# Optimization experiments

Measured on AMD Instinct MI355X. Metric: run time of the kernel, lower is better.

Reference implementation:

```python
import jax, jax.numpy as jnp
import numpy as np
import math

N = 20000      # nodes
E = 640000     # edges (avg degree 32)
G = 128        # g_dim (input features)
H1 = 128       # rgcn output dim
H2 = 128       # transformer output dim
R = 8          # num_relations


def setup_inputs() -> dict:
    key = jax.random.key(0)
    ks = jax.random.split(key, 12)
    x = jax.random.normal(ks[0], (N, G), dtype=jnp.float32)
    edge_index = jax.random.randint(ks[1], (2, E), 0, N)
    edge_type = jax.random.randint(ks[2], (E,), 0, R)
    s_in = 1.0 / math.sqrt(G)
    s_h1 = 1.0 / math.sqrt(H1)
    return {
        'x': x,
        'edge_index': edge_index,
        'edge_type': edge_type,
        # RGCNConv params (per-relation weights + root weight + bias)
        'rgcn_weight': jax.random.normal(ks[3], (R, G, H1), dtype=jnp.float32) * s_in,
        'rgcn_root': jax.random.normal(ks[4], (G, H1), dtype=jnp.float32) * s_in,
        'rgcn_bias': jnp.zeros((H1,), dtype=jnp.float32),
        # TransformerConv params (heads=1): query/key/value + skip linear
        'Wq': jax.random.normal(ks[5], (H1, H2), dtype=jnp.float32) * s_h1,
        'bq': jnp.zeros((H2,), dtype=jnp.float32),
        'Wk': jax.random.normal(ks[6], (H1, H2), dtype=jnp.float32) * s_h1,
        'bk': jnp.zeros((H2,), dtype=jnp.float32),
        'Wv': jax.random.normal(ks[7], (H1, H2), dtype=jnp.float32) * s_h1,
        'bv': jnp.zeros((H2,), dtype=jnp.float32),
        'Ws': jax.random.normal(ks[8], (H1, H2), dtype=jnp.float32) * s_h1,
        'bs': jnp.zeros((H2,), dtype=jnp.float32),
    }


def reference(x, edge_index, edge_type, rgcn_weight, rgcn_root, rgcn_bias,
              Wq, bq, Wk, bk, Wv, bv, Ws, bs):
    n = x.shape[0]
    src, dst = edge_index[0], edge_index[1]

    # ---- RGCNConv (aggr='mean' per relation, root weight + bias) ----
    # transform nodes by every relation, then gather per-edge message
    xr = jnp.einsum('ni,rio->nro', x, rgcn_weight)          # [N, R, H1]
    msg = xr[src, edge_type]                                # [E, H1]
    # per (dst, relation) edge counts for mean aggregation
    cnt = jnp.zeros((n, rgcn_weight.shape[0]), x.dtype).at[dst, edge_type].add(1.0)
    denom = jnp.maximum(cnt[dst, edge_type], 1.0)[:, None]  # [E, 1]
    agg = jnp.zeros((n, rgcn_weight.shape[2]), x.dtype).at[dst].add(msg / denom)
    h = agg + x @ rgcn_root + rgcn_bias
    h = jax.nn.relu(h)

    # ---- TransformerConv (heads=1, concat, root_weight=True) ----
    d = Wq.shape[1]
    q = h @ Wq + bq                                          # [N, H2]
    k = h @ Wk + bk
    v = h @ Wv + bv
    score = jnp.sum(q[dst] * k[src], axis=-1) / math.sqrt(d) # [E]
    # softmax over incoming edges of each destination node
    smax = jax.ops.segment_max(score, dst, num_segments=n)   # [N]
    e = jnp.exp(score - smax[dst])                           # [E]
    den = jax.ops.segment_sum(e, dst, num_segments=n)        # [N]
    alpha = e / jnp.maximum(den[dst], 1e-16)                 # [E]
    out = jax.ops.segment_sum(alpha[:, None] * v[src], dst, num_segments=n)
    out = out + h @ Ws + bs                                  # skip connection
    return jax.nn.relu(out)
```

## Files before the change

kernel.cpp:

```cpp
#include <hip/hip_runtime.h>

typedef unsigned short u16;
typedef unsigned int u32;
typedef __attribute__((ext_vector_type(8))) short short8;
typedef __attribute__((ext_vector_type(4))) float f32x4;

#define NN 20000
#define EE 640000
#define SCAN_BLOCKS 80

__device__ inline u16 f2bf(float f) {
    u32 x = __float_as_uint(f);
    return (u16)((x + 0x7FFFu + ((x >> 16) & 1u)) >> 16);
}
__device__ inline float lo16(u32 w) { return __uint_as_float(w << 16); }
__device__ inline float hi16(u32 w) { return __uint_as_float(w & 0xFFFF0000u); }
__device__ inline u32 packbf(float a, float b) { return ((u32)f2bf(b) << 16) | (u32)f2bf(a); }

__global__ void zero_ints(int* p, int n) {
    int i = blockIdx.x * 256 + threadIdx.x;
    if (i < n) p[i] = 0;
}

__global__ void cast_x(const float* __restrict__ x, u16* __restrict__ xb) {
    int i = blockIdx.x * 256 + threadIdx.x;
    if (i >= NN * 32) return;
    float4 v = *(const float4*)(x + (size_t)i * 4);
    uint2 o;
    o.x = packbf(v.x, v.y);
    o.y = packbf(v.z, v.w);
    *(uint2*)(xb + (size_t)i * 4) = o;
}

__global__ void prep_weights(const float* rw, const float* root,
                             const float* Wq, const float* Wk, const float* Wv, const float* Ws,
                             const float* bq, const float* bk, const float* bv, const float* bs,
                             u16* wt1, u16* wt2, float* bcat) {
    int idx = blockIdx.x * 256 + threadIdx.x;
    const int S1 = 128 * 1152, S2 = 4 * 128 * 128;
    if (idx < S1) {
        int o = idx / 1152, k = idx - o * 1152;
        float v = (k < 1024) ? rw[k * 128 + o] : root[(k - 1024) * 128 + o];
        wt1[idx] = f2bf(v);
    } else if (idx < S1 + S2) {
        int j = idx - S1;
        int y = j >> 14, rem = j & 16383, o = rem >> 7, i = rem & 127;
        const float* W = (y == 0) ? Wq : (y == 1) ? Wk : (y == 2) ? Wv : Ws;
        wt2[j] = f2bf(W[i * 128 + o]);
    } else if (idx < S1 + S2 + 512) {
        int j = idx - (S1 + S2);
        int y = j >> 7, c = j & 127;
        const float* b = (y == 0) ? bq : (y == 1) ? bk : (y == 2) ? bv : bs;
        bcat[j] = b[c];
    }
}

__global__ void count_rank(const int* __restrict__ ei, const int* __restrict__ et,
                           int* __restrict__ cnt, int* __restrict__ rank) {
    int e = blockIdx.x * 256 + threadIdx.x;
    if (e >= EE) return;
    int dst = ei[EE + e];
    int r = et[e];
    rank[e] = atomicAdd(&cnt[dst * 8 + r], 1);
}

__global__ __launch_bounds__(256) void scan_phase1(const int* __restrict__ cnt,
                                                   int* __restrict__ deg_pref,
                                                   int* __restrict__ blk_sums) {
    __shared__ int lds[256];
    int t = threadIdx.x;
    int n = blockIdx.x * 256 + t;
    int d = 0;
    if (n < NN) {
        int4 c0 = *(const int4*)(cnt + n * 8);
        int4 c1 = *(const int4*)(cnt + n * 8 + 4);
        d = c0.x + c0.y + c0.z + c0.w + c1.x + c1.y + c1.z + c1.w;
    }
    lds[t] = d;
    __syncthreads();
    for (int o = 1; o < 256; o <<= 1) {
        int v = (t >= o) ? lds[t - o] : 0;
        __syncthreads();
        lds[t] += v;
        __syncthreads();
    }
    if (n < NN) deg_pref[n] = lds[t];
    if (t == 255) blk_sums[blockIdx.x] = lds[255];
}

__global__ void scan_phase2(int* __restrict__ blk_sums) {
    __shared__ int lds[128];
    int t = threadIdx.x;
    int v = (t < SCAN_BLOCKS) ? blk_sums[t] : 0;
    lds[t] = v;
    __syncthreads();
    for (int o = 1; o < 128; o <<= 1) {
        int a = (t >= o) ? lds[t - o] : 0;
        __syncthreads();
        lds[t] += a;
        __syncthreads();
    }
    if (t < SCAN_BLOCKS) blk_sums[t] = lds[t] - v;
}

__global__ __launch_bounds__(256) void scan_phase3(const int* __restrict__ cnt,
                                                   const int* __restrict__ deg_pref,
                                                   const int* __restrict__ blk_sums,
                                                   int* __restrict__ row_off,
                                                   int* __restrict__ srt) {
    int n = blockIdx.x * 256 + threadIdx.x;
    if (n >= NN) return;
    int4 c0 = *(const int4*)(cnt + n * 8);
    int4 c1 = *(const int4*)(cnt + n * 8 + 4);
    int deg = c0.x + c0.y + c0.z + c0.w + c1.x + c1.y + c1.z + c1.w;
    int start = blk_sums[blockIdx.x] + deg_pref[n] - deg;
    row_off[n] = start;
    int sub = start;
    int o[8];
    o[0] = sub; sub += c0.x;
    o[1] = sub; sub += c0.y;
    o[2] = sub; sub += c0.z;
    o[3] = sub; sub += c0.w;
    o[4] = sub; sub += c1.x;
    o[5] = sub; sub += c1.y;
    o[6] = sub; sub += c1.z;
    o[7] = sub; sub += c1.w;
    *(int4*)(srt + n * 8) = make_int4(o[0], o[1], o[2], o[3]);
    *(int4*)(srt + n * 8 + 4) = make_int4(o[4], o[5], o[6], o[7]);
    if (n == NN - 1) row_off[NN] = sub;
}

__global__ void scatter_kernel(const int* __restrict__ ei, const int* __restrict__ et,
                               const int* __restrict__ srt, const int* __restrict__ rank,
                               int* __restrict__ es) {
    int e = blockIdx.x * 256 + threadIdx.x;
    if (e >= EE) return;
    int dst = ei[EE + e];
    int src = ei[e];
    int r = et[e];
    int pos = srt[dst * 8 + r] + rank[e];
    es[pos] = src;
}

__global__ __launch_bounds__(256) void rgcn_agg(const u16* __restrict__ xb,
                                                const int* __restrict__ srt,
                                                const int* __restrict__ cnt,
                                                const int* __restrict__ es,
                                                u16* __restrict__ pre) {
    int node = blockIdx.x * 8 + (threadIdx.x >> 5);
    int lane = threadIdx.x & 31;
    if (node >= NN) return;
    uint2 xv = *(const uint2*)(xb + (long)node * 128 + lane * 4);
    *(uint2*)(pre + (long)node * 1152 + 1024 + lane * 4) = xv;
#pragma unroll 1
    for (int r = 0; r < 8; r++) {
        int c = cnt[node * 8 + r];
        int p0 = srt[node * 8 + r];
        float inv = 1.0f / (float)(c > 1 ? c : 1);
        float4 a = {0.f, 0.f, 0.f, 0.f};
        int i = 0;
        for (; i + 4 <= c; i += 4) {
            int s0 = es[p0 + i], s1 = es[p0 + i + 1], s2 = es[p0 + i + 2], s3 = es[p0 + i + 3];
            uint2 w0 = *(const uint2*)(xb + (long)s0 * 128 + lane * 4);
            uint2 w1 = *(const uint2*)(xb + (long)s1 * 128 + lane * 4);
            uint2 w2 = *(const uint2*)(xb + (long)s2 * 128 + lane * 4);
            uint2 w3 = *(const uint2*)(xb + (long)s3 * 128 + lane * 4);
            a.x += (lo16(w0.x) + lo16(w1.x)) + (lo16(w2.x) + lo16(w3.x));
            a.y += (hi16(w0.x) + hi16(w1.x)) + (hi16(w2.x) + hi16(w3.x));
            a.z += (lo16(w0.y) + lo16(w1.y)) + (lo16(w2.y) + lo16(w3.y));
            a.w += (hi16(w0.y) + hi16(w1.y)) + (hi16(w2.y) + hi16(w3.y));
        }
        for (; i < c; i++) {
            int s = es[p0 + i];
            uint2 w = *(const uint2*)(xb + (long)s * 128 + lane * 4);
            a.x += lo16(w.x); a.y += hi16(w.x); a.z += lo16(w.y); a.w += hi16(w.y);
        }
        uint2 ow;
        ow.x = packbf(a.x * inv, a.y * inv);
        ow.y = packbf(a.z * inv, a.w * inv);
        *(uint2*)(pre + (long)node * 1152 + r * 128 + lane * 4) = ow;
    }
}

__global__ __launch_bounds__(256) void gemm_kernel(const u16* __restrict__ A, int lda,
                                                   const u16* __restrict__ Bt, int ldbt,
                                                   const float* __restrict__ bias,
                                                   u16* __restrict__ C, int ldc,
                                                   int rows, int K, int relu,
                                                   long long yBt, long long yC, long long yBias) {
    Bt += blockIdx.y * yBt;
    C += blockIdx.y * yC;
    bias += blockIdx.y * yBias;
    __shared__ u16 As[64 * 136];
    __shared__ u16 Bs[128 * 136];
    int tid = threadIdx.x;
    int w = tid >> 6;
    int lane = tid & 63;
    int quad = lane >> 4;
    int ml = lane & 15;
    int block_m = blockIdx.x * 64;

    f32x4 acc[8];
#pragma unroll
    for (int i = 0; i < 8; i++) acc[i] = (f32x4){0.f, 0.f, 0.f, 0.f};

    int rbase = tid >> 4;
    int cb = (tid & 15) * 8;

    for (int kb = 0; kb < K; kb += 128) {
#pragma unroll
        for (int rep = 0; rep < 4; rep++) {
            int r = rbase + rep * 16;
            int gr = block_m + r;
            short8 val = {};
            if (gr < rows) val = *(const short8*)(A + (long)gr * lda + kb + cb);
            *(short8*)(As + r * 136 + cb) = val;
        }
#pragma unroll
        for (int rep = 0; rep < 8; rep++) {
            int r = rbase + rep * 16;
            short8 val = *(const short8*)(Bt + (long)r * ldbt + kb + cb);
            *(short8*)(Bs + r * 136 + cb) = val;
        }
        __syncthreads();
#pragma unroll
        for (int ks = 0; ks < 4; ks++) {
            short8 af = *(const short8*)(As + (w * 16 + ml) * 136 + ks * 32 + quad * 8);
#pragma unroll
            for (int nt = 0; nt < 8; nt++) {
                short8 bfr = *(const short8*)(Bs + (nt * 16 + ml) * 136 + ks * 32 + quad * 8);
                acc[nt] = __builtin_amdgcn_mfma_f32_16x16x32_bf16(af, bfr, acc[nt], 0, 0, 0);
            }
        }
        __syncthreads();
    }
#pragma unroll
    for (int nt = 0; nt < 8; nt++) {
        int col = nt * 16 + ml;
        float bv = bias[col];
#pragma unroll
        for (int i = 0; i < 4; i++) {
            int gr = block_m + w * 16 + quad * 4 + i;
            if (gr < rows) {
                float vv = acc[nt][i] + bv;
                if (relu) vv = fmaxf(vv, 0.f);
                C[(long)gr * ldc + col] = f2bf(vv);
            }
        }
    }
}

__global__ __launch_bounds__(256) void attn_kernel(const u16* __restrict__ q, const u16* __restrict__ k,
                                                   const u16* __restrict__ v, const u16* __restrict__ skip,
                                                   const int* __restrict__ row_off, const int* __restrict__ es,
                                                   float* __restrict__ out) {
    int node = blockIdx.x * 8 + (threadIdx.x >> 5);
    int lane = threadIdx.x & 31;
    if (node >= NN) return;
    int p0 = row_off[node], p1 = row_off[node + 1];
    uint2 qw = *(const uint2*)(q + (long)node * 128 + lane * 4);
    float q0 = lo16(qw.x), q1 = hi16(qw.x), q2 = lo16(qw.y), q3 = hi16(qw.y);
    const float SC = 0.08838834764831845f;
    float m = -INFINITY, l = 0.f;
    float4 a = {0.f, 0.f, 0.f, 0.f};
    int p = p0;
    for (; p + 4 <= p1; p += 4) {
        int s0 = es[p], s1 = es[p + 1], s2 = es[p + 2], s3 = es[p + 3];
        uint2 k0 = *(const uint2*)(k + (long)s0 * 128 + lane * 4);
        uint2 k1 = *(const uint2*)(k + (long)s1 * 128 + lane * 4);
        uint2 k2 = *(const uint2*)(k + (long)s2 * 128 + lane * 4);
        uint2 k3 = *(const uint2*)(k + (long)s3 * 128 + lane * 4);
        uint2 v0 = *(const uint2*)(v + (long)s0 * 128 + lane * 4);
        uint2 v1 = *(const uint2*)(v + (long)s1 * 128 + lane * 4);
        uint2 v2 = *(const uint2*)(v + (long)s2 * 128 + lane * 4);
        uint2 v3 = *(const uint2*)(v + (long)s3 * 128 + lane * 4);
        float t0 = q0 * lo16(k0.x) + q1 * hi16(k0.x) + q2 * lo16(k0.y) + q3 * hi16(k0.y);
        float t1 = q0 * lo16(k1.x) + q1 * hi16(k1.x) + q2 * lo16(k1.y) + q3 * hi16(k1.y);
        float t2 = q0 * lo16(k2.x) + q1 * hi16(k2.x) + q2 * lo16(k2.y) + q3 * hi16(k2.y);
        float t3 = q0 * lo16(k3.x) + q1 * hi16(k3.x) + q2 * lo16(k3.y) + q3 * hi16(k3.y);
#pragma unroll
        for (int off = 16; off >= 1; off >>= 1) {
            t0 += __shfl_xor(t0, off, 32);
            t1 += __shfl_xor(t1, off, 32);
            t2 += __shfl_xor(t2, off, 32);
            t3 += __shfl_xor(t3, off, 32);
        }
        t0 *= SC; t1 *= SC; t2 *= SC; t3 *= SC;
        float mx = fmaxf(fmaxf(t0, t1), fmaxf(t2, t3));
        float mn = fmaxf(m, mx);
        float scale = __expf(m - mn);
        float w0 = __expf(t0 - mn), w1 = __expf(t1 - mn), w2 = __expf(t2 - mn), w3 = __expf(t3 - mn);
        l = l * scale + ((w0 + w1) + (w2 + w3));
        a.x = a.x * scale + w0 * lo16(v0.x) + w1 * lo16(v1.x) + w2 * lo16(v2.x) + w3 * lo16(v3.x);
        a.y = a.y * scale + w0 * hi16(v0.x) + w1 * hi16(v1.x) + w2 * hi16(v2.x) + w3 * hi16(v3.x);
        a.z = a.z * scale + w0 * lo16(v0.y) + w1 * lo16(v1.y) + w2 * lo16(v2.y) + w3 * lo16(v3.y);
        a.w = a.w * scale + w0 * hi16(v0.y) + w1 * hi16(v1.y) + w2 * hi16(v2.y) + w3 * hi16(v3.y);
        m = mn;
    }
    for (; p < p1; p++) {
        int s = es[p];
        uint2 kw = *(const uint2*)(k + (long)s * 128 + lane * 4);
        uint2 vw = *(const uint2*)(v + (long)s * 128 + lane * 4);
        float t = q0 * lo16(kw.x) + q1 * hi16(kw.x) + q2 * lo16(kw.y) + q3 * hi16(kw.y);
#pragma unroll
        for (int off = 16; off >= 1; off >>= 1) t += __shfl_xor(t, off, 32);
        t *= SC;
        float mn = fmaxf(m, t);
        float scale = __expf(m - mn);
        float wgt = __expf(t - mn);
        l = l * scale + wgt;
        a.x = a.x * scale + wgt * lo16(vw.x);
        a.y = a.y * scale + wgt * hi16(vw.x);
        a.z = a.z * scale + wgt * lo16(vw.y);
        a.w = a.w * scale + wgt * hi16(vw.y);
        m = mn;
    }
    float invl = (l > 0.f) ? 1.0f / l : 0.f;
    uint2 sw = *(const uint2*)(skip + (long)node * 128 + lane * 4);
    float4 o4;
    o4.x = fmaxf(a.x * invl + lo16(sw.x), 0.f);
    o4.y = fmaxf(a.y * invl + hi16(sw.x), 0.f);
    o4.z = fmaxf(a.z * invl + lo16(sw.y), 0.f);
    o4.w = fmaxf(a.w * invl + hi16(sw.y), 0.f);
    *(float4*)(out + (long)node * 128 + lane * 4) = o4;
}

extern "C" void kernel_launch(void* const* d_in, const int* in_sizes, int n_in,
                              void* d_out, int out_size, void* d_ws, size_t ws_size,
                              hipStream_t stream) {
    const float* x = (const float*)d_in[0];
    const int* ei = (const int*)d_in[1];
    const int* et = (const int*)d_in[2];
    const float* rw = (const float*)d_in[3];
    const float* root = (const float*)d_in[4];
    const float* rbias = (const float*)d_in[5];
    const float* Wq = (const float*)d_in[6];
    const float* bq = (const float*)d_in[7];
    const float* Wk = (const float*)d_in[8];
    const float* bk = (const float*)d_in[9];
    const float* Wv = (const float*)d_in[10];
    const float* bv = (const float*)d_in[11];
    const float* Ws = (const float*)d_in[12];
    const float* bs = (const float*)d_in[13];

    char* ws = (char*)d_ws;
    size_t off = 0;
    auto alloc = [&](size_t b) {
        size_t o = off;
        off = (off + b + 255) & ~(size_t)255;
        return o;
    };
    u16* pre = (u16*)(ws + alloc((size_t)NN * 1152 * 2));
    u16* h = (u16*)(ws + alloc((size_t)NN * 128 * 2));
    u16* qkvs = (u16*)(ws + alloc((size_t)4 * NN * 128 * 2));
    u16* xb = (u16*)(ws + alloc((size_t)NN * 128 * 2));
    u16* wt1 = (u16*)(ws + alloc((size_t)128 * 1152 * 2));
    u16* wt2 = (u16*)(ws + alloc((size_t)4 * 128 * 128 * 2));
    float* bcat = (float*)(ws + alloc((size_t)512 * 4));
    int* cnt = (int*)(ws + alloc((size_t)NN * 8 * 4));
    int* row_off = (int*)(ws + alloc((size_t)(NN + 1) * 4));
    int* srt = (int*)(ws + alloc((size_t)NN * 8 * 4));
    int* deg_pref = (int*)(ws + alloc((size_t)NN * 4));
    int* blk_sums = (int*)(ws + alloc((size_t)128 * 4));
    int* rank = (int*)(ws + alloc((size_t)EE * 4));
    int* es = (int*)(ws + alloc((size_t)EE * 4));
    (void)ws_size;
    (void)in_sizes;
    (void)n_in;
    (void)out_size;

    zero_ints<<<(NN * 8 + 255) / 256, 256, 0, stream>>>(cnt, NN * 8);

    cast_x<<<(NN * 32 + 255) / 256, 256, 0, stream>>>(x, xb);

    prep_weights<<<(128 * 1152 + 4 * 128 * 128 + 512 + 255) / 256, 256, 0, stream>>>(
        rw, root, Wq, Wk, Wv, Ws, bq, bk, bv, bs, wt1, wt2, bcat);

    count_rank<<<EE / 256, 256, 0, stream>>>(ei, et, cnt, rank);
    scan_phase1<<<SCAN_BLOCKS, 256, 0, stream>>>(cnt, deg_pref, blk_sums);
    scan_phase2<<<1, 128, 0, stream>>>(blk_sums);
    scan_phase3<<<SCAN_BLOCKS, 256, 0, stream>>>(cnt, deg_pref, blk_sums, row_off, srt);
    scatter_kernel<<<EE / 256, 256, 0, stream>>>(ei, et, srt, rank, es);

    rgcn_agg<<<(NN + 7) / 8, 256, 0, stream>>>(xb, srt, cnt, es, pre);

    gemm_kernel<<<dim3((NN + 63) / 64, 1), 256, 0, stream>>>(pre, 1152, wt1, 1152, rbias, h, 128,
                                                             NN, 1152, 1, 0, 0, 0);
    gemm_kernel<<<dim3((NN + 63) / 64, 4), 256, 0, stream>>>(h, 128, wt2, 128, bcat, qkvs, 128,
                                                             NN, 128, 0, (long long)128 * 128,
                                                             (long long)NN * 128, 128);

    attn_kernel<<<(NN + 7) / 8, 256, 0, stream>>>(qkvs, qkvs + (size_t)NN * 128, qkvs + (size_t)2 * NN * 128,
                                                  qkvs + (size_t)3 * NN * 128, row_off, es, (float*)d_out);
}
```

Baseline: 279.1 us.

## Merge prep kernels and parallelize RGCN aggregation per node-relation slot

Fuses the zeroing, x-cast and weight-prep kernels into a single launch to remove two kernel launches. Restructures rgcn_agg so each 16-lane group handles one (node, relation) slot, or the root copy, using 16-byte loads, instead of one 32-lane group looping serially over all 8 relations. This exposes more parallel gather work and wider memory transactions. The cost is more threads issuing duplicate cnt/srt lookups and finer-grained groups with uneven per-slot work.

After: 254.4 us. 8.9% less time.

```diff
diff --git a/kernel.cpp b/kernel.cpp
--- a/kernel.cpp
+++ b/kernel.cpp
@@ -17,26 +17,32 @@
 __device__ inline float hi16(u32 w) { return __uint_as_float(w & 0xFFFF0000u); }
 __device__ inline u32 packbf(float a, float b) { return ((u32)f2bf(b) << 16) | (u32)f2bf(a); }
 
-__global__ void zero_ints(int* p, int n) {
-    int i = blockIdx.x * 256 + threadIdx.x;
-    if (i < n) p[i] = 0;
-}
-
-__global__ void cast_x(const float* __restrict__ x, u16* __restrict__ xb) {
-    int i = blockIdx.x * 256 + threadIdx.x;
-    if (i >= NN * 32) return;
-    float4 v = *(const float4*)(x + (size_t)i * 4);
-    uint2 o;
-    o.x = packbf(v.x, v.y);
-    o.y = packbf(v.z, v.w);
-    *(uint2*)(xb + (size_t)i * 4) = o;
-}
-
-__global__ void prep_weights(const float* rw, const float* root,
-                             const float* Wq, const float* Wk, const float* Wv, const float* Ws,
-                             const float* bq, const float* bk, const float* bv, const float* bs,
-                             u16* wt1, u16* wt2, float* bcat) {
+#define ZP_N (NN * 8)
+#define CX_N (NN * 32)
+#define WP_N (128 * 1152 + 4 * 128 * 128 + 512)
+__global__ __launch_bounds__(256) void prep_all(const float* __restrict__ x,
+                                                const float* rw, const float* root,
+                                                const float* Wq, const float* Wk,
+                                                const float* Wv, const float* Ws,
+                                                const float* bq, const float* bk,
+                                                const float* bv, const float* bs,
+                                                int* __restrict__ cnt, u16* __restrict__ xb,
+                                                u16* wt1, u16* wt2, float* bcat) {
     int idx = blockIdx.x * 256 + threadIdx.x;
+    if (idx < ZP_N) {
+        cnt[idx] = 0;
+        return;
+    }
+    idx -= ZP_N;
+    if (idx < CX_N) {
+        float4 v = *(const float4*)(x + (size_t)idx * 4);
+        uint2 o;
+        o.x = packbf(v.x, v.y);
+        o.y = packbf(v.z, v.w);
+        *(uint2*)(xb + (size_t)idx * 4) = o;
+        return;
+    }
+    idx -= CX_N;
     const int S1 = 128 * 1152, S2 = 4 * 128 * 128;
     if (idx < S1) {
         int o = idx / 1152, k = idx - o * 1152;
@@ -147,39 +153,49 @@
                                                 const int* __restrict__ cnt,
                                                 const int* __restrict__ es,
                                                 u16* __restrict__ pre) {
-    int node = blockIdx.x * 8 + (threadIdx.x >> 5);
-    int lane = threadIdx.x & 31;
-    if (node >= NN) return;
-    uint2 xv = *(const uint2*)(xb + (long)node * 128 + lane * 4);
-    *(uint2*)(pre + (long)node * 1152 + 1024 + lane * 4) = xv;
-#pragma unroll 1
-    for (int r = 0; r < 8; r++) {
-        int c = cnt[node * 8 + r];
-        int p0 = srt[node * 8 + r];
-        float inv = 1.0f / (float)(c > 1 ? c : 1);
-        float4 a = {0.f, 0.f, 0.f, 0.f};
-        int i = 0;
-        for (; i + 4 <= c; i += 4) {
-            int s0 = es[p0 + i], s1 = es[p0 + i + 1], s2 = es[p0 + i + 2], s3 = es[p0 + i + 3];
-            uint2 w0 = *(const uint2*)(xb + (long)s0 * 128 + lane * 4);
-            uint2 w1 = *(const uint2*)(xb + (long)s1 * 128 + lane * 4);
-            uint2 w2 = *(const uint2*)(xb + (long)s2 * 128 + lane * 4);
-            uint2 w3 = *(const uint2*)(xb + (long)s3 * 128 + lane * 4);
-            a.x += (lo16(w0.x) + lo16(w1.x)) + (lo16(w2.x) + lo16(w3.x));
-            a.y += (hi16(w0.x) + hi16(w1.x)) + (hi16(w2.x) + hi16(w3.x));
-            a.z += (lo16(w0.y) + lo16(w1.y)) + (lo16(w2.y) + lo16(w3.y));
-            a.w += (hi16(w0.y) + hi16(w1.y)) + (hi16(w2.y) + hi16(w3.y));
-        }
-        for (; i < c; i++) {
-            int s = es[p0 + i];
-            uint2 w = *(const uint2*)(xb + (long)s * 128 + lane * 4);
-            a.x += lo16(w.x); a.y += hi16(w.x); a.z += lo16(w.y); a.w += hi16(w.y);
-        }
-        uint2 ow;
-        ow.x = packbf(a.x * inv, a.y * inv);
-        ow.y = packbf(a.z * inv, a.w * inv);
-        *(uint2*)(pre + (long)node * 1152 + r * 128 + lane * 4) = ow;
-    }
+    int gid = blockIdx.x * 16 + (threadIdx.x >> 4);
+    int lane = threadIdx.x & 15;
+    if (gid >= NN * 9) return;
+    int node = gid / 9;
+    int slot = gid - node * 9;
+    long prebase = (long)node * 1152;
+    if (slot == 8) {
+        uint4 xv = *(const uint4*)(xb + (long)node * 128 + lane * 8);
+        *(uint4*)(pre + prebase + 1024 + lane * 8) = xv;
+        return;
+    }
+    int c = cnt[node * 8 + slot];
+    int p0 = srt[node * 8 + slot];
+    float inv = 1.0f / (float)(c > 1 ? c : 1);
+    float a0 = 0.f, a1 = 0.f, a2 = 0.f, a3 = 0.f, a4 = 0.f, a5 = 0.f, a6 = 0.f, a7 = 0.f;
+    int i = 0;
+    for (; i + 4 <= c; i += 4) {
+        int s0 = es[p0 + i], s1 = es[p0 + i + 1], s2 = es[p0 + i + 2], s3 = es[p0 + i + 3];
+        uint4 w0 = *(const uint4*)(xb + (long)s0 * 128 + lane * 8);
+        uint4 w1 = *(const uint4*)(xb + (long)s1 * 128 + lane * 8);
+        uint4 w2 = *(const uint4*)(xb + (long)s2 * 128 + lane * 8);
+        uint4 w3 = *(const uint4*)(xb + (long)s3 * 128 + lane * 8);
+        a0 += (lo16(w0.x) + lo16(w1.x)) + (lo16(w2.x) + lo16(w3.x));
+        a1 += (hi16(w0.x) + hi16(w1.x)) + (hi16(w2.x) + hi16(w3.x));
+        a2 += (lo16(w0.y) + lo16(w1.y)) + (lo16(w2.y) + lo16(w3.y));
+        a3 += (hi16(w0.y) + hi16(w1.y)) + (hi16(w2.y) + hi16(w3.y));
+        a4 += (lo16(w0.z) + lo16(w1.z)) + (lo16(w2.z) + lo16(w3.z));
+        a5 += (hi16(w0.z) + hi16(w1.z)) + (hi16(w2.z) + hi16(w3.z));
+        a6 += (lo16(w0.w) + lo16(w1.w)) + (lo16(w2.w) + lo16(w3.w));
+        a7 += (hi16(w0.w) + hi16(w1.w)) + (hi16(w2.w) + hi16(w3.w));
+    }
+    for (; i < c; i++) {
+        int s = es[p0 + i];
+        uint4 w = *(const uint4*)(xb + (long)s * 128 + lane * 8);
+        a0 += lo16(w.x); a1 += hi16(w.x); a2 += lo16(w.y); a3 += hi16(w.y);
+        a4 += lo16(w.z); a5 += hi16(w.z); a6 += lo16(w.w); a7 += hi16(w.w);
+    }
+    uint4 ow;
+    ow.x = packbf(a0 * inv, a1 * inv);
+    ow.y = packbf(a2 * inv, a3 * inv);
+    ow.z = packbf(a4 * inv, a5 * inv);
+    ow.w = packbf(a6 * inv, a7 * inv);
+    *(uint4*)(pre + prebase + slot * 128 + lane * 8) = ow;
 }
 
 __global__ __launch_bounds__(256) void gemm_kernel(const u16* __restrict__ A, int lda,
@@ -369,12 +385,8 @@
     (void)n_in;
     (void)out_size;
 
-    zero_ints<<<(NN * 8 + 255) / 256, 256, 0, stream>>>(cnt, NN * 8);
-
-    cast_x<<<(NN * 32 + 255) / 256, 256, 0, stream>>>(x, xb);
-
-    prep_weights<<<(128 * 1152 + 4 * 128 * 128 + 512 + 255) / 256, 256, 0, stream>>>(
-        rw, root, Wq, Wk, Wv, Ws, bq, bk, bv, bs, wt1, wt2, bcat);
+    prep_all<<<(ZP_N + CX_N + WP_N + 255) / 256, 256, 0, stream>>>(
+        x, rw, root, Wq, Wk, Wv, Ws, bq, bk, bv, bs, cnt, xb, wt1, wt2, bcat);
 
     count_rank<<<EE / 256, 256, 0, stream>>>(ei, et, cnt, rank);
     scan_phase1<<<SCAN_BLOCKS, 256, 0, stream>>>(cnt, deg_pref, blk_sums);
@@ -382,7 +394,7 @@
     scan_phase3<<<SCAN_BLOCKS, 256, 0, stream>>>(cnt, deg_pref, blk_sums, row_off, srt);
     scatter_kernel<<<EE / 256, 256, 0, stream>>>(ei, et, srt, rank, es);
 
-    rgcn_agg<<<(NN + 7) / 8, 256, 0, stream>>>(xb, srt, cnt, es, pre);
+    rgcn_agg<<<(NN * 9 + 15) / 16, 256, 0, stream>>>(xb, srt, cnt, es, pre);
 
     gemm_kernel<<<dim3((NN + 63) / 64, 1), 256, 0, stream>>>(pre, 1152, wt1, 1152, rbias, h, 128,
                                                              NN, 1152, 1, 0, 0, 0);
```
